# Performance work log

Measured on AMD Instinct MI355X. Metric: run time of the kernel, lower is better.

## Reference

```python
import jax, jax.numpy as jnp
import numpy as np

N_NODES = 100000
N_EDGES = 1600000
NFEAT = 256
NHID = 128
NCLASS = 2
NEG_SLOPE = 0.2


def setup_inputs() -> dict:
    key = jax.random.key(0)
    ks = jax.random.split(key, 8)
    x = jax.random.normal(ks[0], (N_NODES, NFEAT), dtype=jnp.float32)
    edge_index = jax.random.randint(ks[1], (2, N_EDGES), 0, N_NODES, dtype=jnp.int64)
    # GATConv params (heads=1): lin weight (no bias), att_src, att_dst, bias
    W = jax.random.normal(ks[2], (NFEAT, NHID), dtype=jnp.float32) * (1.0 / np.sqrt(NFEAT))
    att_src = jax.random.normal(ks[3], (NHID,), dtype=jnp.float32) * (1.0 / np.sqrt(NHID))
    att_dst = jax.random.normal(ks[4], (NHID,), dtype=jnp.float32) * (1.0 / np.sqrt(NHID))
    bias_gat = jnp.zeros((NHID,), dtype=jnp.float32)
    fc_w = jax.random.normal(ks[5], (NCLASS, NHID), dtype=jnp.float32) * (1.0 / np.sqrt(NHID))
    fc_b = jnp.zeros((NCLASS,), dtype=jnp.float32)
    return {"x": x, "edge_index": edge_index, "W": W, "att_src": att_src,
            "att_dst": att_dst, "bias_gat": bias_gat, "fc_w": fc_w, "fc_b": fc_b}


def reference(x, edge_index, W, att_src, att_dst, bias_gat, fc_w, fc_b):
    N = x.shape[0]
    # add self loops (PyG GATConv default)
    loops = jnp.broadcast_to(jnp.arange(N, dtype=edge_index.dtype)[None, :], (2, N))
    ei = jnp.concatenate([edge_index, loops], axis=1)  # [2, E+N]
    src, dst = ei[0], ei[1]

    h = x @ W                                 # [N, NHID]
    a_src = h @ att_src                       # [N]
    a_dst = h @ att_dst                       # [N]

    e = jax.nn.leaky_relu(a_src[src] + a_dst[dst], NEG_SLOPE)  # [E+N]
    # segment softmax over destination nodes (every node has a self loop)
    m = jax.ops.segment_max(e, dst, num_segments=N)
    ex = jnp.exp(e - m[dst])
    s = jax.ops.segment_sum(ex, dst, num_segments=N)
    alpha = ex / (s[dst] + 1e-16)             # [E+N]

    msg = h[src] * alpha[:, None]             # [E+N, NHID]
    out = jax.ops.segment_sum(msg, dst, num_segments=N) + bias_gat  # [N, NHID]

    logits = out @ fc_w.T + fc_b              # [N, NCLASS]
    return jax.nn.log_softmax(logits, axis=1)
```

## Files before the change

kernel.cpp:

```cpp
#include <hip/hip_runtime.h>
#include <hip/hip_bf16.h>
#include <stdint.h>

#define N_NODES 100000
#define N_EDGES 1600000
#define NFEAT   256
#define NHID    128
#define NEG_SLOPE 0.2f

#define NB_B       3125
#define SLAB       1024
#define BIN_BLOCKS 512

typedef __attribute__((ext_vector_type(8))) short short8;
typedef __attribute__((ext_vector_type(4))) float f32x4;

__device__ __forceinline__ int clamp_node(int v) {
    unsigned u = (unsigned)v;
    return (u < (unsigned)N_NODES) ? (int)u : 0;
}

__device__ __forceinline__ unsigned short f2bf(float f) {
    unsigned u = __float_as_uint(f);
    return (unsigned short)((u + 0x7fffu + ((u >> 16) & 1u)) >> 16);
}
__device__ __forceinline__ unsigned pkbf(float a, float b) {
    __hip_bfloat162 t = __float22bfloat162_rn(make_float2(a, b));
    return *reinterpret_cast<unsigned*>(&t);
}
__device__ __forceinline__ float bflo(unsigned p) { return __uint_as_float(p << 16); }
__device__ __forceinline__ float bfhi(unsigned p) { return __uint_as_float(p & 0xffff0000u); }

__global__ __launch_bounds__(256) void k_conv(
    const float* __restrict__ W, unsigned short* __restrict__ Wt)
{
    int id = blockIdx.x * 256 + threadIdx.x;
    int n = id >> 8, k = id & 255;
    Wt[id] = f2bf(W[k * NHID + n]);
}

#define LDS_STRIDE 40
__global__ __launch_bounds__(256) void k_gemm_mfma(
    const float* __restrict__ x,
    const unsigned short* __restrict__ Wt,
    const float* __restrict__ atts,
    const float* __restrict__ attd,
    unsigned short* __restrict__ hb,
    float* __restrict__ asrc,
    float* __restrict__ adst)
{
    __shared__ unsigned short As[128 * LDS_STRIDE];
    __shared__ unsigned short Bs[128 * LDS_STRIDE];
    __shared__ float satt[128][2];

    const int tid  = threadIdx.x;
    const int wave = tid >> 6;
    const int lane = tid & 63;
    const int wm = wave >> 1, wn = wave & 1;
    const int lr = lane & 15, q = lane >> 4;
    const int blockM = blockIdx.x * 128;

    const int sr = tid >> 1;
    const int hh = tid & 1;

    if (tid < 128) { satt[tid][0] = 0.f; satt[tid][1] = 0.f; }

    f32x4 acc[4][4];
#pragma unroll
    for (int a = 0; a < 4; ++a)
#pragma unroll
        for (int b = 0; b < 4; ++b) acc[a][b] = 0.f;

    const int growA = min(blockM + sr, N_NODES - 1);
    const float* xrow = x + (size_t)growA * NFEAT + hh * 16;
    const unsigned short* wrow = Wt + sr * NFEAT + hh * 16;

    float4 va0, va1, va2, va3;
    uint4  vb0, vb1;
    {
        const float4* xp = (const float4*)xrow;
        va0 = xp[0]; va1 = xp[1]; va2 = xp[2]; va3 = xp[3];
        vb0 = *(const uint4*)(wrow);
        vb1 = *(const uint4*)(wrow + 8);
    }

    for (int kt = 0; kt < 8; ++kt) {
        __syncthreads();
        uint4 pa0 = make_uint4(pkbf(va0.x, va0.y), pkbf(va0.z, va0.w),
                               pkbf(va1.x, va1.y), pkbf(va1.z, va1.w));
        uint4 pa1 = make_uint4(pkbf(va2.x, va2.y), pkbf(va2.z, va2.w),
                               pkbf(va3.x, va3.y), pkbf(va3.z, va3.w));
        *(uint4*)&As[sr * LDS_STRIDE + hh * 16 + 0] = pa0;
        *(uint4*)&As[sr * LDS_STRIDE + hh * 16 + 8] = pa1;
        *(uint4*)&Bs[sr * LDS_STRIDE + hh * 16 + 0] = vb0;
        *(uint4*)&Bs[sr * LDS_STRIDE + hh * 16 + 8] = vb1;
        __syncthreads();

        if (kt < 7) {
            const float4* xp = (const float4*)(xrow + (kt + 1) * 32);
            va0 = xp[0]; va1 = xp[1]; va2 = xp[2]; va3 = xp[3];
            vb0 = *(const uint4*)(wrow + (kt + 1) * 32);
            vb1 = *(const uint4*)(wrow + (kt + 1) * 32 + 8);
        }

        short8 af[4], bfr[4];
#pragma unroll
        for (int mt = 0; mt < 4; ++mt)
            af[mt] = *(const short8*)&As[(wm * 64 + mt * 16 + lr) * LDS_STRIDE + q * 8];
#pragma unroll
        for (int nt = 0; nt < 4; ++nt)
            bfr[nt] = *(const short8*)&Bs[(wn * 64 + nt * 16 + lr) * LDS_STRIDE + q * 8];

#pragma unroll
        for (int mt = 0; mt < 4; ++mt)
#pragma unroll
            for (int nt = 0; nt < 4; ++nt)
                acc[mt][nt] = __builtin_amdgcn_mfma_f32_16x16x32_bf16(
                    af[mt], bfr[nt], acc[mt][nt], 0, 0, 0);
    }

    float attsv[4], attdv[4];
#pragma unroll
    for (int nt = 0; nt < 4; ++nt) {
        attsv[nt] = atts[wn * 64 + nt * 16 + lr];
        attdv[nt] = attd[wn * 64 + nt * 16 + lr];
    }
#pragma unroll
    for (int mt = 0; mt < 4; ++mt) {
#pragma unroll
        for (int reg = 0; reg < 4; ++reg) {
            float s = 0.f, d = 0.f;
#pragma unroll
            for (int nt = 0; nt < 4; ++nt) {
                float v = acc[mt][nt][reg];
                s += v * attsv[nt];
                d += v * attdv[nt];
            }
#pragma unroll
            for (int mask = 8; mask > 0; mask >>= 1) {
                s += __shfl_xor(s, mask);
                d += __shfl_xor(d, mask);
            }
            if (lr == 0) {
                int lrow = wm * 64 + mt * 16 + q * 4 + reg;
                atomicAdd(&satt[lrow][0], s);
                atomicAdd(&satt[lrow][1], d);
            }
        }
    }

#pragma unroll
    for (int mt = 0; mt < 4; ++mt) {
#pragma unroll
        for (int reg = 0; reg < 4; ++reg) {
            int grow = blockM + wm * 64 + mt * 16 + q * 4 + reg;
            if (grow < N_NODES) {
                unsigned short* hp = hb + (size_t)grow * NHID + wn * 64 + lr;
#pragma unroll
                for (int nt = 0; nt < 4; ++nt)
                    hp[nt * 16] = f2bf(acc[mt][nt][reg]);
            }
        }
    }

    __syncthreads();
    if (tid < 128) {
        int g = blockM + tid;
        if (g < N_NODES) {
            asrc[g] = satt[tid][0];
            adst[g] = satt[tid][1];
        }
    }
}

__global__ __launch_bounds__(256) void k_bin(
    const int* __restrict__ ei, int* __restrict__ gcur,
    unsigned* __restrict__ staged)
{
    __shared__ int hist[NB_B];
    __shared__ int base[NB_B];
    const int t = threadIdx.x;
    const int per = (N_EDGES + BIN_BLOCKS - 1) / BIN_BLOCKS;
    const int e0 = blockIdx.x * per;
    const int e1 = min(e0 + per, N_EDGES);

    for (int i = t; i < NB_B; i += 256) hist[i] = 0;
    __syncthreads();
    for (int e = e0 + t; e < e1; e += 256)
        atomicAdd(&hist[clamp_node(ei[N_EDGES + e]) >> 5], 1);
    __syncthreads();
    for (int i = t; i < NB_B; i += 256) {
        int c = hist[i];
        base[i] = c ? atomicAdd(&gcur[i], c) : 0;
        hist[i] = 0;
    }
    __syncthreads();
    for (int e = e0 + t; e < e1; e += 256) {
        int d = clamp_node(ei[N_EDGES + e]);
        int s = clamp_node(ei[e]);
        int b = d >> 5;
        int pos = base[b] + atomicAdd(&hist[b], 1);
        if (pos < SLAB)
            staged[(size_t)b * SLAB + pos] = (unsigned)s | ((unsigned)(d & 31) << 17);
    }
}

__global__ __launch_bounds__(256) void k_sort_agg(
    const unsigned* __restrict__ staged, const int* __restrict__ gcur,
    const float* __restrict__ asrc, const float* __restrict__ adst,
    const unsigned short* __restrict__ hb,
    const float* __restrict__ bias, const float* __restrict__ fcw,
    const float* __restrict__ fcb, float* __restrict__ out)
{
    __shared__ float2 buf[SLAB];
    __shared__ int hist[32], scanv[32], cntv[32];
    __shared__ float asrc_s[32], adst_s[32];

    const int b = blockIdx.x;
    const int t = threadIdx.x;
    const int eb = b * SLAB;
    const int n = min(gcur[b], SLAB);
    const int nodeStart = b * 32;

    if (t < 32) {
        hist[t] = 0;
        adst_s[t] = adst[nodeStart + t];
        asrc_s[t] = asrc[nodeStart + t];
    }
    __syncthreads();

    for (int j = t; j < n; j += 256)
        atomicAdd(&hist[(staged[eb + j] >> 17) & 31], 1);
    __syncthreads();

    if (t < 32) {
        int v = hist[t];
        int sc = v;
#pragma unroll
        for (int off = 1; off < 32; off <<= 1) {
            int u = __shfl_up(sc, off);
            if (t >= off) sc += u;
        }
        scanv[t] = sc - v;
        cntv[t] = v;
        hist[t] = 0;
    }
    __syncthreads();

    for (int j = t; j < n; j += 256) {
        unsigned pk = staged[eb + j];
        int s  = pk & 0x1FFFF;
        int dl = (pk >> 17) & 31;
        float a = asrc[s] + adst_s[dl];
        a = (a > 0.f) ? a : NEG_SLOPE * a;
        float ew = __expf(fminf(a, 60.f));
        int pos = scanv[dl] + atomicAdd(&hist[dl], 1);
        buf[pos] = make_float2(__int_as_float(s * 32), ew);
    }
    __syncthreads();

    const int wave = t >> 6;
    const int lane = t & 63;
    const int l5 = lane & 31;
    const int eh = lane >> 5;
    const uint2* hr2 = (const uint2*)hb;

    float b_[4], w0_[4], w1_[4];
#pragma unroll
    for (int k = 0; k < 4; ++k) {
        b_[k]  = bias[4 * l5 + k];
        w0_[k] = fcw[4 * l5 + k];
        w1_[k] = fcw[NHID + 4 * l5 + k];
    }
    const float fb0 = fcb[0], fb1 = fcb[1];

    for (int ln = wave * 8; ln < wave * 8 + 8; ++ln) {
        const int i = nodeStart + ln;
        const int jb = scanv[ln];
        const int nn = cntv[ln];

        float a0 = 0.f, a1 = 0.f, a2 = 0.f, a3 = 0.f;
        for (int j = 0; j < nn; j += 8) {
            float2 m[4]; uint2 p[4]; float ew[4];
#pragma unroll
            for (int u = 0; u < 4; ++u) {
                int e = j + 2 * u + eh;
                int idx = (e < nn) ? e : nn - 1;
                m[u] = buf[jb + idx];
                ew[u] = (e < nn) ? m[u].y : 0.f;
            }
#pragma unroll
            for (int u = 0; u < 4; ++u)
                p[u] = hr2[__float_as_uint(m[u].x) + l5];
#pragma unroll
            for (int u = 0; u < 4; ++u) {
                a0 += ew[u] * bflo(p[u].x);
                a1 += ew[u] * bfhi(p[u].x);
                a2 += ew[u] * bflo(p[u].y);
                a3 += ew[u] * bfhi(p[u].y);
            }
        }
        a0 += __shfl_xor(a0, 32);
        a1 += __shfl_xor(a1, 32);
        a2 += __shfl_xor(a2, 32);
        a3 += __shfl_xor(a3, 32);

        float ss = 0.f;
        for (int jj = lane; jj < nn; jj += 64) ss += buf[jb + jj].y;
#pragma unroll
        for (int off = 32; off > 0; off >>= 1) ss += __shfl_xor(ss, off);

        float e0 = asrc_s[ln] + adst_s[ln];
        e0 = (e0 > 0.f) ? e0 : NEG_SLOPE * e0;
        float w = __expf(fminf(e0, 60.f));
        uint2 pself = hr2[(unsigned)i * 32u + l5];
        a0 += w * bflo(pself.x);
        a1 += w * bfhi(pself.x);
        a2 += w * bflo(pself.y);
        a3 += w * bfhi(pself.y);
        ss += w;

        float inv = 1.0f / (ss + 1e-16f);
        float o0 = a0 * inv + b_[0];
        float o1 = a1 * inv + b_[1];
        float o2 = a2 * inv + b_[2];
        float o3 = a3 * inv + b_[3];

        float l0 = o0 * w0_[0] + o1 * w0_[1] + o2 * w0_[2] + o3 * w0_[3];
        float l1 = o0 * w1_[0] + o1 * w1_[1] + o2 * w1_[2] + o3 * w1_[3];
#pragma unroll
        for (int off = 16; off > 0; off >>= 1) {
            l0 += __shfl_down(l0, off);
            l1 += __shfl_down(l1, off);
        }
        if (lane == 0) {
            l0 += fb0;
            l1 += fb1;
            float m = fmaxf(l0, l1);
            float ls = m + __logf(__expf(l0 - m) + __expf(l1 - m));
            ((float2*)out)[i] = make_float2(l0 - ls, l1 - ls);
        }
    }
}

extern "C" void kernel_launch(void* const* d_in, const int* in_sizes, int n_in,
                              void* d_out, int out_size, void* d_ws, size_t ws_size,
                              hipStream_t stream)
{
    const float* x    = (const float*)d_in[0];
    const int*   ei   = (const int*)d_in[1];
    const float* W    = (const float*)d_in[2];
    const float* atts = (const float*)d_in[3];
    const float* attd = (const float*)d_in[4];
    const float* bias = (const float*)d_in[5];
    const float* fcw  = (const float*)d_in[6];
    const float* fcb  = (const float*)d_in[7];
    float*       out  = (float*)d_out;

    char* base = (char*)d_ws;
    size_t off = 0;
    auto carve = [&](size_t bytes) -> char* {
        char* p = base + off;
        off = (off + bytes + 255) & ~(size_t)255;
        return p;
    };
    unsigned short* hb     = (unsigned short*)carve((size_t)N_NODES * NHID * 2);
    float*          asrc   = (float*)carve(N_NODES * 4);
    float*          adst   = (float*)carve(N_NODES * 4);
    int*            gcur   = (int*)carve(NB_B * 4);
    unsigned*       staged = (unsigned*)carve((size_t)NB_B * SLAB * 4);
    unsigned short* Wt     = (unsigned short*)carve(NHID * NFEAT * 2);
    (void)ws_size; (void)in_sizes; (void)n_in; (void)out_size;

    hipMemsetAsync(gcur, 0, NB_B * 4, stream);

    const int GB = (N_NODES + 127) / 128;

    k_conv<<<(NHID * NFEAT) / 256, 256, 0, stream>>>(W, Wt);
    k_gemm_mfma<<<GB, 256, 0, stream>>>(x, Wt, atts, attd, hb, asrc, adst);
    k_bin<<<BIN_BLOCKS, 256, 0, stream>>>(ei, gcur, staged);
    k_sort_agg<<<NB_B, 256, 0, stream>>>(staged, gcur, asrc, adst, hb,
                                         bias, fcw, fcb, out);
}
```

Before: 318.6 us.

## Split hidden features into two halves aggregated in separate passes

The GEMM now writes h as two separate 64-column bf16 arrays, and aggregation is split into two kernels, one per half. The aim is to shrink the randomly gathered working set per pass so more of it stays in cache. The first pass saves the sorted edge buffer, per-node metadata, softmax sums and partial logits to global memory, and the second pass reloads them and finishes the log-softmax. The cost is an extra kernel launch, extra global traffic for the staged edge buffer, and narrower 4-byte gathers per lane.

```diff
diff --git a/kernel.cpp b/kernel.cpp
--- a/kernel.cpp
+++ b/kernel.cpp
@@ -45,7 +45,8 @@
     const unsigned short* __restrict__ Wt,
     const float* __restrict__ atts,
     const float* __restrict__ attd,
-    unsigned short* __restrict__ hb,
+    unsigned short* __restrict__ hbA,
+    unsigned short* __restrict__ hbB,
     float* __restrict__ asrc,
     float* __restrict__ adst)
 {
@@ -149,13 +150,14 @@
         }
     }
 
+    unsigned short* __restrict__ hbh = wn ? hbB : hbA;
 #pragma unroll
     for (int mt = 0; mt < 4; ++mt) {
 #pragma unroll
         for (int reg = 0; reg < 4; ++reg) {
             int grow = blockM + wm * 64 + mt * 16 + q * 4 + reg;
             if (grow < N_NODES) {
-                unsigned short* hp = hb + (size_t)grow * NHID + wn * 64 + lr;
+                unsigned short* hp = hbh + (size_t)grow * 64 + lr;
 #pragma unroll
                 for (int nt = 0; nt < 4; ++nt)
                     hp[nt * 16] = f2bf(acc[mt][nt][reg]);
@@ -205,12 +207,13 @@
     }
 }
 
-__global__ __launch_bounds__(256) void k_sort_agg(
+__global__ __launch_bounds__(256) void k_aggA(
     const unsigned* __restrict__ staged, const int* __restrict__ gcur,
     const float* __restrict__ asrc, const float* __restrict__ adst,
-    const unsigned short* __restrict__ hb,
+    const unsigned short* __restrict__ hbA,
     const float* __restrict__ bias, const float* __restrict__ fcw,
-    const float* __restrict__ fcb, float* __restrict__ out)
+    float2* __restrict__ bufG, unsigned* __restrict__ metaG,
+    float* __restrict__ ssumG, float2* __restrict__ l01)
 {
     __shared__ float2 buf[SLAB];
     __shared__ int hist[32], scanv[32], cntv[32];
@@ -244,6 +247,7 @@
         scanv[t] = sc - v;
         cntv[t] = v;
         hist[t] = 0;
+        metaG[nodeStart + t] = (unsigned)(sc - v) | ((unsigned)v << 12);
     }
     __syncthreads();
 
@@ -259,29 +263,30 @@
     }
     __syncthreads();
 
+    for (int j = t; j < n; j += 256) bufG[eb + j] = buf[j];
+
     const int wave = t >> 6;
     const int lane = t & 63;
     const int l5 = lane & 31;
     const int eh = lane >> 5;
-    const uint2* hr2 = (const uint2*)hb;
-
-    float b_[4], w0_[4], w1_[4];
-#pragma unroll
-    for (int k = 0; k < 4; ++k) {
-        b_[k]  = bias[4 * l5 + k];
-        w0_[k] = fcw[4 * l5 + k];
-        w1_[k] = fcw[NHID + 4 * l5 + k];
-    }
-    const float fb0 = fcb[0], fb1 = fcb[1];
+    const unsigned* hr = (const unsigned*)hbA;
+
+    float b_[2], w0_[2], w1_[2];
+#pragma unroll
+    for (int k = 0; k < 2; ++k) {
+        b_[k]  = bias[2 * l5 + k];
+        w0_[k] = fcw[2 * l5 + k];
+        w1_[k] = fcw[NHID + 2 * l5 + k];
+    }
 
     for (int ln = wave * 8; ln < wave * 8 + 8; ++ln) {
         const int i = nodeStart + ln;
         const int jb = scanv[ln];
         const int nn = cntv[ln];
 
-        float a0 = 0.f, a1 = 0.f, a2 = 0.f, a3 = 0.f;
+        float a0 = 0.f, a1 = 0.f;
         for (int j = 0; j < nn; j += 8) {
-            float2 m[4]; uint2 p[4]; float ew[4];
+            float2 m[4]; unsigned p[4]; float ew[4];
 #pragma unroll
             for (int u = 0; u < 4; ++u) {
                 int e = j + 2 * u + eh;
@@ -291,19 +296,15 @@
             }
 #pragma unroll
             for (int u = 0; u < 4; ++u)
-                p[u] = hr2[__float_as_uint(m[u].x) + l5];
+                p[u] = hr[__float_as_uint(m[u].x) + l5];
 #pragma unroll
             for (int u = 0; u < 4; ++u) {
-                a0 += ew[u] * bflo(p[u].x);
-                a1 += ew[u] * bfhi(p[u].x);
-                a2 += ew[u] * bflo(p[u].y);
-                a3 += ew[u] * bfhi(p[u].y);
+                a0 += ew[u] * bflo(p[u]);
+                a1 += ew[u] * bfhi(p[u]);
             }
         }
         a0 += __shfl_xor(a0, 32);
         a1 += __shfl_xor(a1, 32);
-        a2 += __shfl_xor(a2, 32);
-        a3 += __shfl_xor(a3, 32);
 
         float ss = 0.f;
         for (int jj = lane; jj < nn; jj += 64) ss += buf[jb + jj].y;
@@ -313,29 +314,125 @@
         float e0 = asrc_s[ln] + adst_s[ln];
         e0 = (e0 > 0.f) ? e0 : NEG_SLOPE * e0;
         float w = __expf(fminf(e0, 60.f));
-        uint2 pself = hr2[(unsigned)i * 32u + l5];
-        a0 += w * bflo(pself.x);
-        a1 += w * bfhi(pself.x);
-        a2 += w * bflo(pself.y);
-        a3 += w * bfhi(pself.y);
+        unsigned pself = hr[(unsigned)i * 32u + l5];
+        a0 += w * bflo(pself);
+        a1 += w * bfhi(pself);
         ss += w;
 
         float inv = 1.0f / (ss + 1e-16f);
         float o0 = a0 * inv + b_[0];
         float o1 = a1 * inv + b_[1];
-        float o2 = a2 * inv + b_[2];
-        float o3 = a3 * inv + b_[3];
-
-        float l0 = o0 * w0_[0] + o1 * w0_[1] + o2 * w0_[2] + o3 * w0_[3];
-        float l1 = o0 * w1_[0] + o1 * w1_[1] + o2 * w1_[2] + o3 * w1_[3];
+
+        float l0 = o0 * w0_[0] + o1 * w0_[1];
+        float l1 = o0 * w1_[0] + o1 * w1_[1];
 #pragma unroll
         for (int off = 16; off > 0; off >>= 1) {
             l0 += __shfl_down(l0, off);
             l1 += __shfl_down(l1, off);
         }
         if (lane == 0) {
-            l0 += fb0;
-            l1 += fb1;
+            ssumG[i] = ss;
+            l01[i] = make_float2(l0, l1);
+        }
+    }
+}
+
+__global__ __launch_bounds__(256) void k_aggB(
+    const int* __restrict__ gcur,
+    const float* __restrict__ asrc, const float* __restrict__ adst,
+    const unsigned short* __restrict__ hbB,
+    const float* __restrict__ bias, const float* __restrict__ fcw,
+    const float* __restrict__ fcb,
+    const float2* __restrict__ bufG, const unsigned* __restrict__ metaG,
+    const float* __restrict__ ssumG, const float2* __restrict__ l01,
+    float* __restrict__ out)
+{
+    __shared__ float2 buf[SLAB];
+    __shared__ int scanv[32], cntv[32];
+    __shared__ float asrc_s[32], adst_s[32], ssum_s[32];
+
+    const int b = blockIdx.x;
+    const int t = threadIdx.x;
+    const int eb = b * SLAB;
+    const int n = min(gcur[b], SLAB);
+    const int nodeStart = b * 32;
+
+    if (t < 32) {
+        unsigned mv = metaG[nodeStart + t];
+        scanv[t] = (int)(mv & 0xFFFu);
+        cntv[t]  = (int)(mv >> 12);
+        adst_s[t] = adst[nodeStart + t];
+        asrc_s[t] = asrc[nodeStart + t];
+        ssum_s[t] = ssumG[nodeStart + t];
+    }
+    for (int j = t; j < n; j += 256) buf[j] = bufG[eb + j];
+    __syncthreads();
+
+    const int wave = t >> 6;
+    const int lane = t & 63;
+    const int l5 = lane & 31;
+    const int eh = lane >> 5;
+    const unsigned* hr = (const unsigned*)hbB;
+
+    float b_[2], w0_[2], w1_[2];
+#pragma unroll
+    for (int k = 0; k < 2; ++k) {
+        b_[k]  = bias[64 + 2 * l5 + k];
+        w0_[k] = fcw[64 + 2 * l5 + k];
+        w1_[k] = fcw[NHID + 64 + 2 * l5 + k];
+    }
+    const float fb0 = fcb[0], fb1 = fcb[1];
+
+    for (int ln = wave * 8; ln < wave * 8 + 8; ++ln) {
+        const int i = nodeStart + ln;
+        const int jb = scanv[ln];
+        const int nn = cntv[ln];
+
+        float a0 = 0.f, a1 = 0.f;
+        for (int j = 0; j < nn; j += 8) {
+            float2 m[4]; unsigned p[4]; float ew[4];
+#pragma unroll
+            for (int u = 0; u < 4; ++u) {
+                int e = j + 2 * u + eh;
+                int idx = (e < nn) ? e : nn - 1;
+                m[u] = buf[jb + idx];
+                ew[u] = (e < nn) ? m[u].y : 0.f;
+            }
+#pragma unroll
+            for (int u = 0; u < 4; ++u)
+                p[u] = hr[__float_as_uint(m[u].x) + l5];
+#pragma unroll
+            for (int u = 0; u < 4; ++u) {
+                a0 += ew[u] * bflo(p[u]);
+                a1 += ew[u] * bfhi(p[u]);
+            }
+        }
+        a0 += __shfl_xor(a0, 32);
+        a1 += __shfl_xor(a1, 32);
+
+        float e0 = asrc_s[ln] + adst_s[ln];
+        e0 = (e0 > 0.f) ? e0 : NEG_SLOPE * e0;
+        float w = __expf(fminf(e0, 60.f));
+        unsigned pself = hr[(unsigned)i * 32u + l5];
+        a0 += w * bflo(pself);
+        a1 += w * bfhi(pself);
+        float ss = ssum_s[ln];
+
+        float inv = 1.0f / (ss + 1e-16f);
+        float o0 = a0 * inv + b_[0];
+        float o1 = a1 * inv + b_[1];
+
+        float l0 = o0 * w0_[0] + o1 * w0_[1];
+        float l1 = o0 * w1_[0] + o1 * w1_[1];
+#pragma unroll
+        for (int off = 16; off > 0; off >>= 1) {
+            l0 += __shfl_down(l0, off);
+            l1 += __shfl_down(l1, off);
+        }
+        if (lane == 0) {
+            float2 part = l01[i];
+            l0 += part.x + fb0;
+            l1 += part.y + fb1;
             float m = fmaxf(l0, l1);
             float ls = m + __logf(__expf(l0 - m) + __expf(l1 - m));
             ((float2*)out)[i] = make_float2(l0 - ls, l1 - ls);
@@ -364,11 +461,16 @@
         off = (off + bytes + 255) & ~(size_t)255;
         return p;
     };
-    unsigned short* hb     = (unsigned short*)carve((size_t)N_NODES * NHID * 2);
+    unsigned short* hbA    = (unsigned short*)carve((size_t)N_NODES * 64 * 2);
+    unsigned short* hbB    = (unsigned short*)carve((size_t)N_NODES * 64 * 2);
     float*          asrc   = (float*)carve(N_NODES * 4);
     float*          adst   = (float*)carve(N_NODES * 4);
     int*            gcur   = (int*)carve(NB_B * 4);
     unsigned*       staged = (unsigned*)carve((size_t)NB_B * SLAB * 4);
+    float2*         bufG   = (float2*)carve((size_t)NB_B * SLAB * 8);
+    unsigned*       metaG  = (unsigned*)carve(N_NODES * 4);
+    float*          ssumG  = (float*)carve(N_NODES * 4);
+    float2*         l01    = (float2*)carve(N_NODES * 8);
     unsigned short* Wt     = (unsigned short*)carve(NHID * NFEAT * 2);
     (void)ws_size; (void)in_sizes; (void)n_in; (void)out_size;
 
@@ -377,8 +479,10 @@
     const int GB = (N_NODES + 127) / 128;
 
     k_conv<<<(NHID * NFEAT) / 256, 256, 0, stream>>>(W, Wt);
-    k_gemm_mfma<<<GB, 256, 0, stream>>>(x, Wt, atts, attd, hb, asrc, adst);
+    k_gemm_mfma<<<GB, 256, 0, stream>>>(x, Wt, atts, attd, hbA, hbB, asrc, adst);
     k_bin<<<BIN_BLOCKS, 256, 0, stream>>>(ei, gcur, staged);
-    k_sort_agg<<<NB_B, 256, 0, stream>>>(staged, gcur, asrc, adst, hb,
-                                         bias, fcw, fcb, out);
-}
+    k_aggA<<<NB_B, 256, 0, stream>>>(staged, gcur, asrc, adst, hbA,
+                                     bias, fcw, bufG, metaG, ssumG, l01);
+    k_aggB<<<NB_B, 256, 0, stream>>>(gcur, asrc, adst, hbB, bias, fcw, fcb,
+                                     bufG, metaG, ssumG, l01, out);
+}
```

After: 349.7 us. +9.8%, slower.
